# Kernel tuning notes

Hardware: AMD Instinct MI355X
Metric: run time of the kernel (lower is better)

## Reference

```python
import jax, jax.numpy as jnp
import numpy as np

D_MODEL = 2048
N_HEADS = 16
HEAD_DIM = D_MODEL // N_HEADS
D_FF = 4 * D_MODEL
BATCH = 2
SEQ = 2048
LN_EPS = 1e-5


def setup_inputs() -> dict:
    key = jax.random.key(0)
    ks = jax.random.split(key, 12)
    s = 0.02
    return {
        "x": jax.random.normal(ks[0], (BATCH, SEQ, D_MODEL), dtype=jnp.float32),
        "alibi_bias": jax.random.normal(ks[1], (N_HEADS, SEQ, SEQ), dtype=jnp.float32),
        "W_q": jax.random.normal(ks[2], (D_MODEL, D_MODEL), dtype=jnp.float32) * s,
        "W_k": jax.random.normal(ks[3], (D_MODEL, D_MODEL), dtype=jnp.float32) * s,
        "W_v": jax.random.normal(ks[4], (D_MODEL, D_MODEL), dtype=jnp.float32) * s,
        "W_o": jax.random.normal(ks[5], (D_MODEL, D_MODEL), dtype=jnp.float32) * s,
        "ln1_g": jnp.ones((D_MODEL,), dtype=jnp.float32),
        "ln1_b": jnp.zeros((D_MODEL,), dtype=jnp.float32),
        "ln2_g": jnp.ones((D_MODEL,), dtype=jnp.float32),
        "ln2_b": jnp.zeros((D_MODEL,), dtype=jnp.float32),
        "ffn_w1": jax.random.normal(ks[6], (D_MODEL, D_FF), dtype=jnp.float32) * s,
        "ffn_b1": jnp.zeros((D_FF,), dtype=jnp.float32),
        "ffn_w2": jax.random.normal(ks[7], (D_FF, D_MODEL), dtype=jnp.float32) * s,
        "ffn_b2": jnp.zeros((D_MODEL,), dtype=jnp.float32),
    }


def _layernorm(x, g, b):
    mu = jnp.mean(x, axis=-1, keepdims=True)
    var = jnp.mean(jnp.square(x - mu), axis=-1, keepdims=True)
    return (x - mu) * jax.lax.rsqrt(var + LN_EPS) * g + b


def _mha(x, alibi_bias, W_q, W_k, W_v, W_o):
    B, S, _ = x.shape
    # nn.Linear applies x @ W.T; here W_* are stored as (in, out) so plain matmul.
    q = (x @ W_q).reshape(B, S, N_HEADS, HEAD_DIM).transpose(0, 2, 1, 3)
    k = (x @ W_k).reshape(B, S, N_HEADS, HEAD_DIM).transpose(0, 2, 1, 3)
    v = (x @ W_v).reshape(B, S, N_HEADS, HEAD_DIM).transpose(0, 2, 1, 3)
    q = q / np.sqrt(HEAD_DIM).astype(np.float32)
    scores = jnp.einsum("bhqd,bhkd->bhqk", q, k)  # [B,H,S,S]
    scores = scores + alibi_bias[None]
    causal = jnp.triu(jnp.ones((S, S), dtype=bool), k=1)
    scores = jnp.where(causal, jnp.finfo(scores.dtype).min, scores)
    attn = jax.nn.softmax(scores, axis=-1)
    out = jnp.einsum("bhqk,bhkd->bhqd", attn, v)
    out = out.transpose(0, 2, 1, 3).reshape(B, S, D_MODEL)
    return out @ W_o


def reference(x, alibi_bias, W_q, W_k, W_v, W_o, ln1_g, ln1_b, ln2_g, ln2_b,
              ffn_w1, ffn_b1, ffn_w2, ffn_b2):
    # Attention block (pre-LN, residual); dropout is identity in eval mode.
    h = x + _mha(_layernorm(x, ln1_g, ln1_b), alibi_bias, W_q, W_k, W_v, W_o)
    # FFN block
    n2 = _layernorm(h, ln2_g, ln2_b)
    ffn = jax.nn.gelu(n2 @ ffn_w1 + ffn_b1, approximate=False) @ ffn_w2 + ffn_b2
    return h + ffn
```

## Files before the change

### kernel.cpp

```cpp
#include <hip/hip_runtime.h>
#include <math.h>

#define DM   2048
#define DFF  8192
#define NH   16
#define HD   128
#define SEQ  2048
#define MROWS 4096

typedef __attribute__((ext_vector_type(4))) float  f32x4;
typedef __attribute__((ext_vector_type(8))) __bf16 bf16x8;
typedef __attribute__((ext_vector_type(4))) short  short4_t;

#define VMCNT(n) asm volatile("s_waitcnt vmcnt(" #n ")" ::: "memory")
#define LGKM0()  asm volatile("s_waitcnt lgkmcnt(0)" ::: "memory")
#define SBAR()   asm volatile("s_barrier" ::: "memory")
#define SCHEDB() __builtin_amdgcn_sched_barrier(0)

__device__ inline unsigned short f2bf(float f) {
  union { float f; unsigned int u; } x; x.f = f;
  unsigned int r = x.u + 0x7FFFu + ((x.u >> 16) & 1u);
  return (unsigned short)(r >> 16);
}

__device__ inline void gload16(const void* g, void* l) {
  __builtin_amdgcn_global_load_lds(
      (const __attribute__((address_space(1))) unsigned int*)g,
      (__attribute__((address_space(3))) unsigned int*)l, 16, 0, 0);
}

__global__ __launch_bounds__(256) void ln_kernel(
    const float* __restrict__ in, const float* __restrict__ gw,
    const float* __restrict__ bw, unsigned short* __restrict__ out)
{
  const int row = blockIdx.x;
  const float* xr = in + (size_t)row * DM;
  const int t = threadIdx.x, lane = t & 63, w = t >> 6;
  float4 v0 = ((const float4*)xr)[t];
  float4 v1 = ((const float4*)xr)[t + 256];
  float s = v0.x+v0.y+v0.z+v0.w + v1.x+v1.y+v1.z+v1.w;
  float s2 = v0.x*v0.x+v0.y*v0.y+v0.z*v0.z+v0.w*v0.w
           + v1.x*v1.x+v1.y*v1.y+v1.z*v1.z+v1.w*v1.w;
  #pragma unroll
  for (int off = 32; off; off >>= 1) { s += __shfl_xor(s, off); s2 += __shfl_xor(s2, off); }
  __shared__ float rs[4], rs2[4];
  if (lane == 0) { rs[w] = s; rs2[w] = s2; }
  __syncthreads();
  s = rs[0] + rs[1] + rs[2] + rs[3];
  s2 = rs2[0] + rs2[1] + rs2[2] + rs2[3];
  const float mu = s * (1.0f / DM);
  const float var = s2 * (1.0f / DM) - mu * mu;
  const float rstd = rsqrtf(var + 1e-5f);
  float4 g0 = ((const float4*)gw)[t],     b0 = ((const float4*)bw)[t];
  float4 g1 = ((const float4*)gw)[t+256], b1 = ((const float4*)bw)[t+256];
  unsigned short* o = out + (size_t)row * DM;
  int i0 = t * 4, i1 = (t + 256) * 4;
  o[i0+0] = f2bf((v0.x-mu)*rstd*g0.x + b0.x);
  o[i0+1] = f2bf((v0.y-mu)*rstd*g0.y + b0.y);
  o[i0+2] = f2bf((v0.z-mu)*rstd*g0.z + b0.z);
  o[i0+3] = f2bf((v0.w-mu)*rstd*g0.w + b0.w);
  o[i1+0] = f2bf((v1.x-mu)*rstd*g1.x + b1.x);
  o[i1+1] = f2bf((v1.y-mu)*rstd*g1.y + b1.y);
  o[i1+2] = f2bf((v1.z-mu)*rstd*g1.z + b1.z);
  o[i1+3] = f2bf((v1.w-mu)*rstd*g1.w + b1.w);
}

__global__ void transpose_kernel(const float* __restrict__ in,
                                 unsigned short* __restrict__ out,
                                 int nrows, int ncols)
{
  __shared__ float tile[32][33];
  const int bx = blockIdx.x * 32;
  const int by = blockIdx.y * 32;
  const int tx = threadIdx.x, ty = threadIdx.y;
  #pragma unroll
  for (int i = ty; i < 32; i += 8)
    tile[i][tx] = in[(size_t)(by + i) * ncols + bx + tx];
  __syncthreads();
  #pragma unroll
  for (int i = ty; i < 32; i += 8)
    out[(size_t)(bx + i) * nrows + by + tx] = f2bf(tile[tx][i]);
}

enum { EP_Q = 0, EP_K = 1, EP_V = 2, EP_WO = 3, EP_FFN1 = 4, EP_FFN2 = 5 };

#define QUAD(MH, NH)                                                                   \
  do {                                                                                 \
    __builtin_amdgcn_s_setprio(1);                                                     \
    acc[MH][NH][0][0] = __builtin_amdgcn_mfma_f32_16x16x32_bf16(a[0][0], b[NH][0][0], acc[MH][NH][0][0], 0, 0, 0); \
    acc[MH][NH][0][0] = __builtin_amdgcn_mfma_f32_16x16x32_bf16(a[0][1], b[NH][0][1], acc[MH][NH][0][0], 0, 0, 0); \
    acc[MH][NH][0][1] = __builtin_amdgcn_mfma_f32_16x16x32_bf16(a[0][0], b[NH][1][0], acc[MH][NH][0][1], 0, 0, 0); \
    acc[MH][NH][0][1] = __builtin_amdgcn_mfma_f32_16x16x32_bf16(a[0][1], b[NH][1][1], acc[MH][NH][0][1], 0, 0, 0); \
    acc[MH][NH][1][0] = __builtin_amdgcn_mfma_f32_16x16x32_bf16(a[1][0], b[NH][0][0], acc[MH][NH][1][0], 0, 0, 0); \
    acc[MH][NH][1][0] = __builtin_amdgcn_mfma_f32_16x16x32_bf16(a[1][1], b[NH][0][1], acc[MH][NH][1][0], 0, 0, 0); \
    acc[MH][NH][1][1] = __builtin_amdgcn_mfma_f32_16x16x32_bf16(a[1][0], b[NH][1][0], acc[MH][NH][1][1], 0, 0, 0); \
    acc[MH][NH][1][1] = __builtin_amdgcn_mfma_f32_16x16x32_bf16(a[1][1], b[NH][1][1], acc[MH][NH][1][1], 0, 0, 0); \
    __builtin_amdgcn_s_setprio(0);                                                     \
  } while (0)

template <int MODE>
__global__ __launch_bounds__(512, 2) void gemm_kernel(
    const unsigned short* __restrict__ A,
    const unsigned short* __restrict__ Bt,
    int K, int N,
    const float* __restrict__ res,
    const float* __restrict__ bias,
    void* __restrict__ out)
{
  __shared__ unsigned short lds[2][3][8192];

  const int t = threadIdx.x;
  const int w = t >> 6, lane = t & 63;
  const int wm = w >> 2, wn = w & 3;
  const int c = lane & 15, g = lane >> 4;
  const int l3 = lane >> 3, l7 = lane & 7;
  const int cs = c & 7;

  const long bm = (long)blockIdx.x * 128;
  const long bn = (long)blockIdx.y * 256;
  const int NT = K >> 6;
  const size_t Ksz = (size_t)K;

  const int scol = (l7 ^ l3) * 8;
  const int r0a = w * 16;

  auto stA = [&](int T) {
    unsigned short* d = &lds[T & 1][0][r0a * 64];
    #pragma unroll
    for (int j = 0; j < 2; j++)
      gload16(A + (bm + r0a + j * 8 + l3) * Ksz + T * 64 + scol, d + j * 512);
  };
  auto stB = [&](int T, int nh) {
    unsigned short* d = &lds[T & 1][1 + nh][r0a * 64];
    #pragma unroll
    for (int j = 0; j < 2; j++)
      gload16(Bt + (bn + nh * 128 + r0a + j * 8 + l3) * Ksz + T * 64 + scol, d + j * 512);
  };

  f32x4 acc[2][2][2][2];
  #pragma unroll
  for (int i = 0; i < 2; i++)
    #pragma unroll
    for (int jq = 0; jq < 2; jq++)
      #pragma unroll
      for (int m = 0; m < 2; m++)
        #pragma unroll
        for (int n = 0; n < 2; n++) acc[i][jq][m][n] = (f32x4){0.f, 0.f, 0.f, 0.f};

  stB(0, 0); stB(0, 1); stA(0);
  stB(1, 0); stB(1, 1); stA(1);
  VMCNT(6);
  SBAR();

  const int arow = (wm * 64 + c) * 64;
  const int brow = (wn * 32 + c) * 64;
  const int k0o = (g ^ cs) * 8;
  const int k1o = ((4 | g) ^ cs) * 8;

  for (int T = 0; T < NT; T++) {
    const unsigned short* LA  = lds[T & 1][0];
    const unsigned short* LB0 = lds[T & 1][1];
    const unsigned short* LB1 = lds[T & 1][2];
    bf16x8 a[2][2], b[2][2][2];

    a[0][0] = *(const bf16x8*)&LA[arow + k0o];
    a[0][1] = *(const bf16x8*)&LA[arow + k1o];
    a[1][0] = *(const bf16x8*)&LA[arow + 1024 + k0o];
    a[1][1] = *(const bf16x8*)&LA[arow + 1024 + k1o];
    b[0][0][0] = *(const bf16x8*)&LB0[brow + k0o];
    b[0][0][1] = *(const bf16x8*)&LB0[brow + k1o];
    b[0][1][0] = *(const bf16x8*)&LB0[brow + 1024 + k0o];
    b[0][1][1] = *(const bf16x8*)&LB0[brow + 1024 + k1o];
    SBAR();
    LGKM0(); SCHEDB();
    QUAD(0, 0);
    SBAR();

    b[1][0][0] = *(const bf16x8*)&LB1[brow + k0o];
    b[1][0][1] = *(const bf16x8*)&LB1[brow + k1o];
    b[1][1][0] = *(const bf16x8*)&LB1[brow + 1024 + k0o];
    b[1][1][1] = *(const bf16x8*)&LB1[brow + 1024 + k1o];
    if (T + 2 < NT) stB(T + 2, 0);
    SBAR();
    LGKM0(); SCHEDB();
    QUAD(0, 1);
    SBAR();

    a[0][0] = *(const bf16x8*)&LA[arow + 2048 + k0o];
    a[0][1] = *(const bf16x8*)&LA[arow + 2048 + k1o];
    a[1][0] = *(const bf16x8*)&LA[arow + 3072 + k0o];
    a[1][1] = *(const bf16x8*)&LA[arow + 3072 + k1o];
    if (T + 2 < NT) stB(T + 2, 1);
    SBAR();
    LGKM0(); SCHEDB();
    QUAD(1, 0);
    SBAR();

    if (T + 2 < NT) stA(T + 2);
    QUAD(1, 1);
    if (T + 2 < NT) { VMCNT(6); } else { VMCNT(0); }
    SBAR();
  }

  #pragma unroll
  for (int mh = 0; mh < 2; mh++)
    #pragma unroll
    for (int nh = 0; nh < 2; nh++)
      #pragma unroll
      for (int m = 0; m < 2; m++)
        #pragma unroll
        for (int n = 0; n < 2; n++) {
          const long row0 = bm + wm * 64 + mh * 32 + m * 16 + g * 4;
          const long col  = bn + nh * 128 + wn * 32 + n * 16 + c;
          #pragma unroll
          for (int r = 0; r < 4; r++) {
            const long row = row0 + r;
            float v = acc[mh][nh][m][n][r];
            if constexpr (MODE == EP_Q) {
              ((unsigned short*)out)[(((row >> 11) * NH + (col >> 7)) * (long)SEQ + (row & 2047)) * HD + (col & 127)] =
                  f2bf(v * 0.08838834764831845f);
            } else if constexpr (MODE == EP_K) {
              ((unsigned short*)out)[(((row >> 11) * NH + (col >> 7)) * (long)SEQ + (row & 2047)) * HD + (col & 127)] = f2bf(v);
            } else if constexpr (MODE == EP_V) {
              ((unsigned short*)out)[(((row >> 11) * NH + (col >> 7)) * (long)HD + (col & 127)) * SEQ + (row & 2047)] = f2bf(v);
            } else if constexpr (MODE == EP_WO) {
              ((float*)out)[row * DM + col] = res[row * DM + col] + v;
            } else if constexpr (MODE == EP_FFN1) {
              float u = v + bias[col];
              float y = 0.7978845608028654f * (u + 0.044715f * u * u * u);
              float e = __expf(-2.0f * fabsf(y));
              float th = (1.0f - e) / (1.0f + e);
              th = (y < 0.0f) ? -th : th;
              ((unsigned short*)out)[row * (long)N + col] = f2bf(0.5f * u * (1.0f + th));
            } else {
              ((float*)out)[row * DM + col] = res[row * DM + col] + v + bias[col];
            }
          }
        }
}

__global__ __launch_bounds__(256) void attn_kernel(
    const unsigned short* __restrict__ Q,
    const unsigned short* __restrict__ Kg,
    const unsigned short* __restrict__ Vt,
    const float* __restrict__ alibi,
    unsigned short* __restrict__ Out)
{
  __shared__ unsigned short lds[2][16384];

  const int bh = blockIdx.x;
  const int h = bh & (NH - 1);
  const int b = bh >> 4;
  const int j = blockIdx.y;
  const int t = threadIdx.x;
  const int w = t >> 6;
  const int lane = t & 63;
  const int c = lane & 15, g = lane >> 4;
  const int cx = (c & 7) << 4;

  const char* KpB = (const char*)(Kg + (size_t)bh * SEQ * HD);
  const char* VpB = (const char*)(Vt + (size_t)bh * SEQ * HD);
  const unsigned short* Qp = Q + (size_t)bh * SEQ * HD;
  const float* Ah = alibi + (size_t)h * SEQ * SEQ;

  #pragma unroll 1
  for (int half = 0; half < 2; half++) {
    const int cidx = half ? (31 - j) : j;
    const int nt = cidx + 1;
    const int qb = cidx * 64;
    const int q0 = qb + w * 16, qc = q0 + c;

    bf16x8 qf[4];
    #pragma unroll
    for (int dt = 0; dt < 4; dt++)
      qf[dt] = *(const bf16x8*)(Qp + (size_t)qc * HD + dt * 32 + g * 8);

    f32x4 oacc[8];
    #pragma unroll
    for (int d = 0; d < 8; d++) oacc[d] = (f32x4){0.f, 0.f, 0.f, 0.f};
    float m_run = -1e30f, s_run = 0.f;
    const float* Ap = Ah + (size_t)qc * SEQ;

    auto stage = [&](int tt, unsigned short* dst) {
      const size_t kvo = (size_t)tt * 64;
      #pragma unroll
      for (int k = 0; k < 8; k++) {
        const int o = w * 8192 + k * 1024 + lane * 16;
        if (w < 2) {
          const int so = o ^ (((o >> 8) & 7) << 4);
          gload16(KpB + kvo * 256 + so, dst + ((w * 8192 + k * 1024) >> 1));
        } else {
          const int o2 = o - 16384;
          const int d = o2 >> 7, win = o2 & 127;
          gload16(VpB + (size_t)d * 4096 + kvo * 2 + (win ^ ((d & 7) << 4)),
                  dst + ((w * 8192 + k * 1024) >> 1));
        }
      }
    };

    stage(0, lds[0]);
    __syncthreads();
    int buf = 0;

    for (int tt = 0; tt < nt; tt++) {
      if (tt + 1 < nt) stage(tt + 1, lds[buf ^ 1]);
      const unsigned short* LK = lds[buf];
      const unsigned short* LV = lds[buf] + 8192;
      const int kv0 = tt * 64;

      f32x4 sc[4];
      #pragma unroll
      for (int st = 0; st < 4; st++) sc[st] = (f32x4){0.f, 0.f, 0.f, 0.f};
      #pragma unroll
      for (int dt = 0; dt < 4; dt++)
        #pragma unroll
        for (int st = 0; st < 4; st++) {
          bf16x8 kf = *(const bf16x8*)&LK[(st * 4096 + c * 256 + ((dt * 64 + g * 16) ^ cx)) >> 1];
          sc[st] = __builtin_amdgcn_mfma_f32_16x16x32_bf16(kf, qf[dt], sc[st], 0, 0, 0);
        }

      float4 al[4];
      #pragma unroll
      for (int st = 0; st < 4; st++) al[st] = *(const float4*)(Ap + kv0 + st * 16 + g * 4);
      float scr[16];
      #pragma unroll
      for (int st = 0; st < 4; st++) {
        scr[st*4+0] = (kv0 + st*16 + g*4 + 0 > qc) ? -1e30f : sc[st][0] + al[st].x;
        scr[st*4+1] = (kv0 + st*16 + g*4 + 1 > qc) ? -1e30f : sc[st][1] + al[st].y;
        scr[st*4+2] = (kv0 + st*16 + g*4 + 2 > qc) ? -1e30f : sc[st][2] + al[st].z;
        scr[st*4+3] = (kv0 + st*16 + g*4 + 3 > qc) ? -1e30f : sc[st][3] + al[st].w;
      }

      float tm = scr[0];
      #pragma unroll
      for (int i = 1; i < 16; i++) tm = fmaxf(tm, scr[i]);
      tm = fmaxf(tm, __shfl_xor(tm, 16));
      tm = fmaxf(tm, __shfl_xor(tm, 32));
      const float m_new = fmaxf(m_run, tm);
      const float corr = __expf(m_run - m_new);
      float pv[16]; float ps = 0.f;
      #pragma unroll
      for (int i = 0; i < 16; i++) { pv[i] = __expf(scr[i] - m_new); ps += pv[i]; }
      ps += __shfl_xor(ps, 16);
      ps += __shfl_xor(ps, 32);
      s_run = s_run * corr + ps;
      m_run = m_new;

      short4_t pf[4];
      #pragma unroll
      for (int st = 0; st < 4; st++) {
        pf[st][0] = (short)f2bf(pv[st*4+0]); pf[st][1] = (short)f2bf(pv[st*4+1]);
        pf[st][2] = (short)f2bf(pv[st*4+2]); pf[st][3] = (short)f2bf(pv[st*4+3]);
      }

      float cf[4];
      #pragma unroll
      for (int r = 0; r < 4; r++) cf[r] = __shfl(corr, g * 4 + r);

      #pragma unroll
      for (int dt = 0; dt < 8; dt++) {
        f32x4 o = oacc[dt];
        o[0] *= cf[0]; o[1] *= cf[1]; o[2] *= cf[2]; o[3] *= cf[3];
        #pragma unroll
        for (int st = 0; st < 4; st++) {
          short4_t vf = *(const short4_t*)&LV[((dt * 16 + c) * 128 + ((st * 32 + g * 8) ^ cx)) >> 1];
          o = __builtin_amdgcn_mfma_f32_16x16x16bf16_1k(pf[st], vf, o, 0, 0, 0);
        }
        oacc[dt] = o;
      }

      __syncthreads();
      buf ^= 1;
    }

    float inv[4];
    #pragma unroll
    for (int r = 0; r < 4; r++) inv[r] = 1.0f / __shfl(s_run, g * 4 + r);
    #pragma unroll
    for (int dt = 0; dt < 8; dt++)
      #pragma unroll
      for (int r = 0; r < 4; r++)
        Out[(size_t)(b * SEQ + q0 + g * 4 + r) * DM + h * HD + dt * 16 + c] =
            f2bf(oacc[dt][r] * inv[r]);
  }
}

extern "C" void kernel_launch(void* const* d_in, const int* in_sizes, int n_in,
                              void* d_out, int out_size, void* d_ws, size_t ws_size,
                              hipStream_t stream) {
  const float* x     = (const float*)d_in[0];
  const float* alibi = (const float*)d_in[1];
  const float* Wq    = (const float*)d_in[2];
  const float* Wk    = (const float*)d_in[3];
  const float* Wv    = (const float*)d_in[4];
  const float* Wo    = (const float*)d_in[5];
  const float* ln1g  = (const float*)d_in[6];
  const float* ln1b  = (const float*)d_in[7];
  const float* ln2g  = (const float*)d_in[8];
  const float* ln2b  = (const float*)d_in[9];
  const float* w1    = (const float*)d_in[10];
  const float* b1    = (const float*)d_in[11];
  const float* w2    = (const float*)d_in[12];
  const float* b2    = (const float*)d_in[13];

  char* ws = (char*)d_ws;
  float*          hbuf = (float*)(ws);
  unsigned short* xn   = (unsigned short*)(ws + (32ull  << 20));
  unsigned short* qb   = (unsigned short*)(ws + (48ull  << 20));
  unsigned short* kb   = (unsigned short*)(ws + (64ull  << 20));
  unsigned short* vt   = (unsigned short*)(ws + (80ull  << 20));
  unsigned short* ao   = (unsigned short*)(ws + (96ull  << 20));
  unsigned short* wt   = (unsigned short*)(ws + (112ull << 20));
  unsigned short* a1   = (unsigned short*)(ws + (48ull  << 20));

  dim3 blk256(256);
  dim3 blk512(512);
  dim3 tb(32, 8);

  ln_kernel<<<MROWS, blk256, 0, stream>>>(x, ln1g, ln1b, xn);

  transpose_kernel<<<dim3(DM/32, DM/32), tb, 0, stream>>>(Wq, wt, DM, DM);
  gemm_kernel<EP_Q><<<dim3(MROWS/128, DM/256), blk512, 0, stream>>>(xn, wt, DM, DM, nullptr, nullptr, qb);
  transpose_kernel<<<dim3(DM/32, DM/32), tb, 0, stream>>>(Wk, wt, DM, DM);
  gemm_kernel<EP_K><<<dim3(MROWS/128, DM/256), blk512, 0, stream>>>(xn, wt, DM, DM, nullptr, nullptr, kb);
  transpose_kernel<<<dim3(DM/32, DM/32), tb, 0, stream>>>(Wv, wt, DM, DM);
  gemm_kernel<EP_V><<<dim3(MROWS/128, DM/256), blk512, 0, stream>>>(xn, wt, DM, DM, nullptr, nullptr, vt);

  attn_kernel<<<dim3(NH * 2, 16), blk256, 0, stream>>>(qb, kb, vt, alibi, ao);

  transpose_kernel<<<dim3(DM/32, DM/32), tb, 0, stream>>>(Wo, wt, DM, DM);
  gemm_kernel<EP_WO><<<dim3(MROWS/128, DM/256), blk512, 0, stream>>>(ao, wt, DM, DM, x, nullptr, hbuf);

  ln_kernel<<<MROWS, blk256, 0, stream>>>(hbuf, ln2g, ln2b, xn);

  transpose_kernel<<<dim3(DFF/32, DM/32), tb, 0, stream>>>(w1, wt, DM, DFF);
  gemm_kernel<EP_FFN1><<<dim3(MROWS/128, DFF/256), blk512, 0, stream>>>(xn, wt, DM, DFF, nullptr, b1, a1);

  transpose_kernel<<<dim3(DM/32, DFF/32), tb, 0, stream>>>(w2, wt, DFF, DM);
  gemm_kernel<EP_FFN2><<<dim3(MROWS/128, DM/256), blk512, 0, stream>>>(a1, wt, DFF, DM, hbuf, b2, (float*)d_out);
}
```

Measured before the change: 686.6 us.

## Fuse Q/K/V projections into one GEMM and batch weight transposes

Replaces the three separate Q, K and V GEMM launches with one GEMM over a concatenated 3*DM-wide transposed weight. The epilogue routes each column slot to the Q (scaled), K or V-transposed output layout. The four attention weight transposes are merged into a single launch with a z-dimension, and the Wo GEMM reads its slice from that buffer. The GEMM main loop is also restructured: all A fragments are loaded once per K-step and the global prefetch order changes (B half for T+1, then A and B0 for T+2), with matching vmcnt waits. This aims to cut launch count, improve wave quantization for the QKV projection and reduce LDS reads, at the cost of a larger weight workspace and a pipeline that must be exactly right.

```diff
diff --git a/kernel.cpp b/kernel.cpp
--- a/kernel.cpp
+++ b/kernel.cpp
@@ -82,21 +82,29 @@
     out[(size_t)(bx + i) * nrows + by + tx] = f2bf(tile[tx][i]);
 }
 
-enum { EP_Q = 0, EP_K = 1, EP_V = 2, EP_WO = 3, EP_FFN1 = 4, EP_FFN2 = 5 };
-
-#define QUAD(MH, NH)                                                                   \
-  do {                                                                                 \
-    __builtin_amdgcn_s_setprio(1);                                                     \
-    acc[MH][NH][0][0] = __builtin_amdgcn_mfma_f32_16x16x32_bf16(a[0][0], b[NH][0][0], acc[MH][NH][0][0], 0, 0, 0); \
-    acc[MH][NH][0][0] = __builtin_amdgcn_mfma_f32_16x16x32_bf16(a[0][1], b[NH][0][1], acc[MH][NH][0][0], 0, 0, 0); \
-    acc[MH][NH][0][1] = __builtin_amdgcn_mfma_f32_16x16x32_bf16(a[0][0], b[NH][1][0], acc[MH][NH][0][1], 0, 0, 0); \
-    acc[MH][NH][0][1] = __builtin_amdgcn_mfma_f32_16x16x32_bf16(a[0][1], b[NH][1][1], acc[MH][NH][0][1], 0, 0, 0); \
-    acc[MH][NH][1][0] = __builtin_amdgcn_mfma_f32_16x16x32_bf16(a[1][0], b[NH][0][0], acc[MH][NH][1][0], 0, 0, 0); \
-    acc[MH][NH][1][0] = __builtin_amdgcn_mfma_f32_16x16x32_bf16(a[1][1], b[NH][0][1], acc[MH][NH][1][0], 0, 0, 0); \
-    acc[MH][NH][1][1] = __builtin_amdgcn_mfma_f32_16x16x32_bf16(a[1][0], b[NH][1][0], acc[MH][NH][1][1], 0, 0, 0); \
-    acc[MH][NH][1][1] = __builtin_amdgcn_mfma_f32_16x16x32_bf16(a[1][1], b[NH][1][1], acc[MH][NH][1][1], 0, 0, 0); \
-    __builtin_amdgcn_s_setprio(0);                                                     \
-  } while (0)
+__global__ void transpose4_kernel(const float* __restrict__ w0,
+                                  const float* __restrict__ w1,
+                                  const float* __restrict__ w2,
+                                  const float* __restrict__ w3,
+                                  unsigned short* __restrict__ out)
+{
+  __shared__ float tile[32][33];
+  const float* srcs[4] = {w0, w1, w2, w3};
+  const float* in = srcs[blockIdx.z];
+  unsigned short* o = out + (size_t)blockIdx.z * DM * DM;
+  const int bx = blockIdx.x * 32;
+  const int by = blockIdx.y * 32;
+  const int tx = threadIdx.x, ty = threadIdx.y;
+  #pragma unroll
+  for (int i = ty; i < 32; i += 8)
+    tile[i][tx] = in[(size_t)(by + i) * DM + bx + tx];
+  __syncthreads();
+  #pragma unroll
+  for (int i = ty; i < 32; i += 8)
+    o[(size_t)(bx + i) * DM + by + tx] = f2bf(tile[tx][i]);
+}
+
+enum { EP_QKV = 0, EP_WO = 3, EP_FFN1 = 4, EP_FFN2 = 5 };
 
 template <int MODE>
 __global__ __launch_bounds__(512, 2) void gemm_kernel(
@@ -147,9 +155,9 @@
         #pragma unroll
         for (int n = 0; n < 2; n++) acc[i][jq][m][n] = (f32x4){0.f, 0.f, 0.f, 0.f};
 
-  stB(0, 0); stB(0, 1); stA(0);
-  stB(1, 0); stB(1, 1); stA(1);
-  VMCNT(6);
+  stA(0); stB(0, 0); stB(0, 1);
+  stA(1); stB(1, 0);
+  VMCNT(4);
   SBAR();
 
   const int arow = (wm * 64 + c) * 64;
@@ -161,44 +169,56 @@
     const unsigned short* LA  = lds[T & 1][0];
     const unsigned short* LB0 = lds[T & 1][1];
     const unsigned short* LB1 = lds[T & 1][2];
-    bf16x8 a[2][2], b[2][2][2];
-
-    a[0][0] = *(const bf16x8*)&LA[arow + k0o];
-    a[0][1] = *(const bf16x8*)&LA[arow + k1o];
-    a[1][0] = *(const bf16x8*)&LA[arow + 1024 + k0o];
-    a[1][1] = *(const bf16x8*)&LA[arow + 1024 + k1o];
-    b[0][0][0] = *(const bf16x8*)&LB0[brow + k0o];
-    b[0][0][1] = *(const bf16x8*)&LB0[brow + k1o];
-    b[0][1][0] = *(const bf16x8*)&LB0[brow + 1024 + k0o];
-    b[0][1][1] = *(const bf16x8*)&LB0[brow + 1024 + k1o];
+    bf16x8 a[2][2][2], b[2][2];
+
+    #pragma unroll
+    for (int mh = 0; mh < 2; mh++)
+      #pragma unroll
+      for (int m = 0; m < 2; m++) {
+        a[mh][m][0] = *(const bf16x8*)&LA[arow + mh * 2048 + m * 1024 + k0o];
+        a[mh][m][1] = *(const bf16x8*)&LA[arow + mh * 2048 + m * 1024 + k1o];
+      }
+    #pragma unroll
+    for (int n = 0; n < 2; n++) {
+      b[n][0] = *(const bf16x8*)&LB0[brow + n * 1024 + k0o];
+      b[n][1] = *(const bf16x8*)&LB0[brow + n * 1024 + k1o];
+    }
+    if (T + 1 < NT) stB(T + 1, 1);
     SBAR();
     LGKM0(); SCHEDB();
-    QUAD(0, 0);
+    __builtin_amdgcn_s_setprio(1);
+    #pragma unroll
+    for (int kk = 0; kk < 2; kk++)
+      #pragma unroll
+      for (int mh = 0; mh < 2; mh++)
+        #pragma unroll
+        for (int m = 0; m < 2; m++)
+          #pragma unroll
+          for (int n = 0; n < 2; n++)
+            acc[mh][0][m][n] = __builtin_amdgcn_mfma_f32_16x16x32_bf16(a[mh][m][kk], b[n][kk], acc[mh][0][m][n], 0, 0, 0);
+    __builtin_amdgcn_s_setprio(0);
     SBAR();
 
-    b[1][0][0] = *(const bf16x8*)&LB1[brow + k0o];
-    b[1][0][1] = *(const bf16x8*)&LB1[brow + k1o];
-    b[1][1][0] = *(const bf16x8*)&LB1[brow + 1024 + k0o];
-    b[1][1][1] = *(const bf16x8*)&LB1[brow + 1024 + k1o];
-    if (T + 2 < NT) stB(T + 2, 0);
+    #pragma unroll
+    for (int n = 0; n < 2; n++) {
+      b[n][0] = *(const bf16x8*)&LB1[brow + n * 1024 + k0o];
+      b[n][1] = *(const bf16x8*)&LB1[brow + n * 1024 + k1o];
+    }
+    if (T + 2 < NT) { stA(T + 2); stB(T + 2, 0); }
     SBAR();
     LGKM0(); SCHEDB();
-    QUAD(0, 1);
-    SBAR();
-
-    a[0][0] = *(const bf16x8*)&LA[arow + 2048 + k0o];
-    a[0][1] = *(const bf16x8*)&LA[arow + 2048 + k1o];
-    a[1][0] = *(const bf16x8*)&LA[arow + 3072 + k0o];
-    a[1][1] = *(const bf16x8*)&LA[arow + 3072 + k1o];
-    if (T + 2 < NT) stB(T + 2, 1);
-    SBAR();
-    LGKM0(); SCHEDB();
-    QUAD(1, 0);
-    SBAR();
-
-    if (T + 2 < NT) stA(T + 2);
-    QUAD(1, 1);
-    if (T + 2 < NT) { VMCNT(6); } else { VMCNT(0); }
+    __builtin_amdgcn_s_setprio(1);
+    #pragma unroll
+    for (int kk = 0; kk < 2; kk++)
+      #pragma unroll
+      for (int mh = 0; mh < 2; mh++)
+        #pragma unroll
+        for (int m = 0; m < 2; m++)
+          #pragma unroll
+          for (int n = 0; n < 2; n++)
+            acc[mh][1][m][n] = __builtin_amdgcn_mfma_f32_16x16x32_bf16(a[mh][m][kk], b[n][kk], acc[mh][1][m][n], 0, 0, 0);
+    __builtin_amdgcn_s_setprio(0);
+    if (T + 2 < NT) { VMCNT(4); } else { VMCNT(0); }
     SBAR();
   }
 
@@ -216,13 +236,18 @@
           for (int r = 0; r < 4; r++) {
             const long row = row0 + r;
             float v = acc[mh][nh][m][n][r];
-            if constexpr (MODE == EP_Q) {
-              ((unsigned short*)out)[(((row >> 11) * NH + (col >> 7)) * (long)SEQ + (row & 2047)) * HD + (col & 127)] =
-                  f2bf(v * 0.08838834764831845f);
-            } else if constexpr (MODE == EP_K) {
-              ((unsigned short*)out)[(((row >> 11) * NH + (col >> 7)) * (long)SEQ + (row & 2047)) * HD + (col & 127)] = f2bf(v);
-            } else if constexpr (MODE == EP_V) {
-              ((unsigned short*)out)[(((row >> 11) * NH + (col >> 7)) * (long)HD + (col & 127)) * SEQ + (row & 2047)] = f2bf(v);
+            if constexpr (MODE == EP_QKV) {
+              const int slot = (int)(col >> 11);
+              const long cc = col & 2047;
+              const long hh = cc >> 7, dd = cc & 127;
+              const long bb = row >> 11, ss = row & 2047;
+              unsigned short* o = (unsigned short*)out;
+              if (slot == 0)
+                o[((bb * NH + hh) * SEQ + ss) * HD + dd] = f2bf(v * 0.08838834764831845f);
+              else if (slot == 1)
+                o[8388608 + ((bb * NH + hh) * SEQ + ss) * HD + dd] = f2bf(v);
+              else
+                o[16777216 + ((bb * NH + hh) * HD + dd) * SEQ + ss] = f2bf(v);
             } else if constexpr (MODE == EP_WO) {
               ((float*)out)[row * DM + col] = res[row * DM + col] + v;
             } else if constexpr (MODE == EP_FFN1) {
@@ -419,17 +444,15 @@
 
   ln_kernel<<<MROWS, blk256, 0, stream>>>(x, ln1g, ln1b, xn);
 
-  transpose_kernel<<<dim3(DM/32, DM/32), tb, 0, stream>>>(Wq, wt, DM, DM);
-  gemm_kernel<EP_Q><<<dim3(MROWS/128, DM/256), blk512, 0, stream>>>(xn, wt, DM, DM, nullptr, nullptr, qb);
-  transpose_kernel<<<dim3(DM/32, DM/32), tb, 0, stream>>>(Wk, wt, DM, DM);
-  gemm_kernel<EP_K><<<dim3(MROWS/128, DM/256), blk512, 0, stream>>>(xn, wt, DM, DM, nullptr, nullptr, kb);
-  transpose_kernel<<<dim3(DM/32, DM/32), tb, 0, stream>>>(Wv, wt, DM, DM);
-  gemm_kernel<EP_V><<<dim3(MROWS/128, DM/256), blk512, 0, stream>>>(xn, wt, DM, DM, nullptr, nullptr, vt);
+  transpose4_kernel<<<dim3(DM/32, DM/32, 4), tb, 0, stream>>>(Wq, Wk, Wv, Wo, wt);
+
+  gemm_kernel<EP_QKV><<<dim3(MROWS/128, (3*DM)/256), blk512, 0, stream>>>(
+      xn, wt, DM, 3*DM, nullptr, nullptr, qb);
 
   attn_kernel<<<dim3(NH * 2, 16), blk256, 0, stream>>>(qb, kb, vt, alibi, ao);
 
-  transpose_kernel<<<dim3(DM/32, DM/32), tb, 0, stream>>>(Wo, wt, DM, DM);
-  gemm_kernel<EP_WO><<<dim3(MROWS/128, DM/256), blk512, 0, stream>>>(ao, wt, DM, DM, x, nullptr, hbuf);
+  gemm_kernel<EP_WO><<<dim3(MROWS/128, DM/256), blk512, 0, stream>>>(
+      ao, wt + 3ull * DM * DM, DM, DM, x, nullptr, hbuf);
 
   ln_kernel<<<MROWS, blk256, 0, stream>>>(hbuf, ln2g, ln2b, xn);
 
```

New measurement: 703.4 us. +2.5%, slower.
